# Kernel tuning notes

Hardware: AMD Instinct MI355X
Metric: run time of the kernel (lower is better)

## Reference

```python
import jax, jax.numpy as jnp
import numpy as np
from jax import lax

EPS = 2e-05


def _conv2d(x, w, b, stride):
    # x: [B,C,H,W], w: [O,I,3,3] (OIHW), VALID padding
    y = lax.conv_general_dilated(x, w, (stride, stride), 'VALID',
                                 dimension_numbers=('NCHW', 'OIHW', 'NCHW'))
    return y + b[None, :, None, None]


def _reflect_pad(x):
    return jnp.pad(x, ((0, 0), (0, 0), (1, 1), (1, 1)), mode='reflect')


def _transfer(cont_feat, styl_feat):
    # cont_feat, styl_feat: [B, N, H, W]
    B, N, H, W = cont_feat.shape
    xc = cont_feat.reshape(B, N, -1)   # [B,N,Mc]
    xs = styl_feat.reshape(B, N, -1)   # [B,N,Ms]
    I = jnp.eye(N, dtype=xc.dtype)

    # whitening of content
    mc = jnp.mean(xc, axis=-1, keepdims=True)
    xc0 = xc - mc
    cov_c = jnp.einsum('bnm,bkm->bnk', xc0, xc0) / (xc0.shape[-1] - 1)
    Lc = jnp.linalg.cholesky(cov_c + EPS * I)  # eps*I regularization (torch retry loop)
    inv_Lc = jnp.linalg.inv(Lc)
    whiten = jnp.einsum('bnk,bkm->bnm', inv_Lc, xc0)

    # coloring with style statistics
    ms = jnp.mean(xs, axis=-1, keepdims=True)
    xs0 = xs - ms
    cov_s = jnp.einsum('bnm,bkm->bnk', xs0, xs0) / (xs0.shape[-1] - 1)
    Ls = jnp.linalg.cholesky(cov_s + EPS * I)
    colored = jnp.einsum('bnk,bkm->bnm', Ls, whiten) + ms
    return colored.reshape(B, N, H, W)


def setup_inputs() -> dict:
    key = jax.random.key(0)
    k1, k2, k3, k4 = jax.random.split(key, 4)
    B, C, H, W = 8, 128, 256, 256
    cont_feat = jax.random.normal(k1, (B, C, H, W), dtype=jnp.float32)
    styl_feat = jax.random.normal(k2, (B, C, H, W), dtype=jnp.float32)
    # conv params (kaiming-ish scaling)
    fan1 = C * 9
    W1 = jax.random.normal(k3, (C, C, 3, 3), dtype=jnp.float32) / np.sqrt(fan1)
    b1 = jnp.zeros((C,), dtype=jnp.float32)
    W2 = jax.random.normal(k4, (2 * C, C, 3, 3), dtype=jnp.float32) / np.sqrt(fan1)
    b2 = jnp.zeros((2 * C,), dtype=jnp.float32)
    return {'cont_feat': cont_feat, 'styl_feat': styl_feat,
            'W1': W1, 'b1': b1, 'W2': W2, 'b2': b2}


def reference(cont_feat, styl_feat, W1, b1, W2, b2):
    cs = _transfer(cont_feat, styl_feat)          # [B,C,H,W]
    x = _conv2d(_reflect_pad(cs), W1, b1, 2)      # [B,C,H/2,W/2]
    x = jax.nn.relu(x)
    out = _conv2d(_reflect_pad(x), W2, b2, 1)     # [B,2C,H/2,W/2]
    return out
```

## Files before the change

kernel.cpp:

```cpp
#include <hip/hip_runtime.h>
#include <hip/hip_bf16.h>

#define B_  8
#define C_  128
#define M_  65536
#define EPSV 2e-05f

typedef __attribute__((ext_vector_type(8))) short bf16x8;
typedef __attribute__((ext_vector_type(4))) float f32x4;

#define MFMA(a, b, c) __builtin_amdgcn_mfma_f32_16x16x32_bf16((a), (b), (c), 0, 0, 0)

__device__ __forceinline__ short f2b(float f) {
    unsigned u = __float_as_uint(f);
    u = (u + 0x7FFFu + ((u >> 16) & 1u)) >> 16;
    return (short)u;
}

__device__ __forceinline__ int swz(int px, int c) {
    return px * 256 + ((((c >> 3) ^ (px & 15)) << 4) | ((c & 7) << 1));
}

__device__ __forceinline__ int rot(int i, int k) {
    return i * 128 + ((((k >> 2) + i) & 31) << 2) + (k & 3);
}

__global__ __launch_bounds__(256) void k_prep(const float* W1, const float* W2,
                                              short* wp1, short* wp2) {
    int idx = blockIdx.x * 256 + threadIdx.x;
    if (idx < 9 * 128 * 128) {
        int c = idx & 127, o = (idx >> 7) & 127, rs = idx >> 14;
        wp1[idx] = f2b(W1[(o * 128 + c) * 9 + rs]);
    }
    idx -= 9 * 128 * 128;
    if (idx >= 0 && idx < 9 * 256 * 128) {
        int c = idx & 127, o = (idx >> 7) & 255, rs = idx >> 15;
        wp2[idx] = f2b(W2[(o * 128 + c) * 9 + rs]);
    }
}

__global__ __launch_bounds__(256, 2) void k_gram(const float* cont, const float* styl,
                                                 float* G, float* S) {
    __shared__ short ls[128 * 136];
    __shared__ float ssum[128 * 32];
    int bx = blockIdx.x;
    int chunk = bx & 31, which = (bx >> 5) & 1, b = bx >> 6;
    const float* X = (which ? styl : cont) + (size_t)b * C_ * M_ + chunk * 2048;
    int tid = threadIdx.x, lane = tid & 63, wid = tid >> 6;
    int kg = tid & 31, r0 = tid >> 5;

    float sacc[16];
    #pragma unroll
    for (int p = 0; p < 16; ++p) sacc[p] = 0.f;
    f32x4 acc[2][8];
    for (int u = 0; u < 2; ++u)
        for (int j = 0; j < 8; ++j) acc[u][j] = (f32x4){0.f, 0.f, 0.f, 0.f};

    float4 pf[16];
    #pragma unroll
    for (int p = 0; p < 16; ++p)
        pf[p] = *(const float4*)(X + (size_t)(r0 + p * 8) * M_ + kg * 4);

    for (int it = 0; it < 16; ++it) {
        #pragma unroll
        for (int p = 0; p < 16; ++p) {
            int row = r0 + p * 8;
            float4 v = pf[p];
            sacc[p] += v.x + v.y + v.z + v.w;
            union { __hip_bfloat162 h[2]; unsigned long long u; } pk;
            pk.h[0] = __float22bfloat162_rn(make_float2(v.x, v.y));
            pk.h[1] = __float22bfloat162_rn(make_float2(v.z, v.w));
            *(unsigned long long*)(ls + row * 136 + kg * 4) = pk.u;
        }
        if (it < 15) {
            int kb = (it + 1) * 128;
            #pragma unroll
            for (int p = 0; p < 16; ++p)
                pf[p] = *(const float4*)(X + (size_t)(r0 + p * 8) * M_ + kb + kg * 4);
        }
        asm volatile("s_waitcnt lgkmcnt(0)" ::: "memory");
        __builtin_amdgcn_sched_barrier(0);
        __builtin_amdgcn_s_barrier();
        for (int ks = 0; ks < 4; ++ks) {
            int co = ks * 32 + (lane >> 4) * 8;
            bf16x8 a[2], bbf[8];
            for (int u = 0; u < 2; ++u) {
                int row = (wid * 2 + u) * 16 + (lane & 15);
                a[u] = *(const bf16x8*)(ls + row * 136 + co);
            }
            for (int j = 0; j < 8; ++j) {
                int row = j * 16 + (lane & 15);
                bbf[j] = *(const bf16x8*)(ls + row * 136 + co);
            }
            for (int u = 0; u < 2; ++u)
                for (int j = 0; j < 8; ++j)
                    acc[u][j] = MFMA(a[u], bbf[j], acc[u][j]);
        }
        __builtin_amdgcn_sched_barrier(0);
        __builtin_amdgcn_s_barrier();
    }
    __syncthreads();
    for (int p = 0; p < 16; ++p) ssum[(r0 + p * 8) * 32 + kg] = sacc[p];
    __syncthreads();
    float* Gp = G + ((size_t)which * 8 + b) * 16384;
    float* Sp = S + ((size_t)which * 8 + b) * 128;
    if (tid < 128) {
        float s = 0.f;
        for (int q = 0; q < 32; ++q) s += ssum[tid * 32 + q];
        atomicAdd(&Sp[tid], s);
    }
    for (int u = 0; u < 2; ++u) {
        int rowb = (wid * 2 + u) * 16 + (lane >> 4) * 4;
        for (int j = 0; j < 8; ++j) {
            int col = j * 16 + (lane & 15);
            for (int e = 0; e < 4; ++e)
                atomicAdd(&Gp[(rowb + e) * 128 + col], acc[u][j][e]);
        }
    }
}

__global__ __launch_bounds__(128) void k_chol(const float* G, const float* S,
                                              float* LcT, float* Lsg) {
    __shared__ float A[128 * 128];
    int wb = blockIdx.x;
    int i = threadIdx.x;
    const float invM = 1.f / 65536.f;
    const float invM1 = 1.f / 65535.f;
    const float* Gp = G + (size_t)wb * 16384;
    const float* Sp = S + (size_t)wb * 128;
    float mui = Sp[i] * invM;

    for (int j = 0; j <= i; ++j) {
        float muj = Sp[j] * invM;
        float cv = (Gp[i * 128 + j] - 65536.f * mui * muj) * invM1;
        if (j == i) cv += EPSV;
        A[rot(i, j)] = cv;
    }
    for (int bb = 0; bb < 4; ++bb) {
        int jb0 = bb * 32, bend = jb0 + 32;
        for (int j = jb0; j < bend; ++j) {
            __syncthreads();
            float dot = 0.f;
            if (i >= j) {
                int c0 = jb0 >> 2, c1 = j >> 2;
                float4 dd = {0.f, 0.f, 0.f, 0.f};
                for (int c = c0; c < c1; ++c) {
                    float4 x = *(const float4*)(A + i * 128 + (((c + i) & 31) << 2));
                    float4 y = *(const float4*)(A + j * 128 + (((c + j) & 31) << 2));
                    dd.x += x.x * y.x; dd.y += x.y * y.y;
                    dd.z += x.z * y.z; dd.w += x.w * y.w;
                }
                dot = dd.x + dd.y + dd.z + dd.w;
                for (int k = c1 << 2; k < j; ++k)
                    dot += A[rot(i, k)] * A[rot(j, k)];
            }
            if (i == j) A[127] = sqrtf(A[rot(i, j)] - dot);
            __syncthreads();
            if (i > j)       A[rot(i, j)] = (A[rot(i, j)] - dot) / A[127];
            else if (i == j) A[rot(i, j)] = A[127];
        }
        if (bb < 3) {
            __syncthreads();
            if (i >= bend) {
                float t[32];
                #pragma unroll
                for (int g = 0; g < 8; ++g) {
                    float4 v = *(const float4*)(A + i * 128 +
                                ((((jb0 >> 2) + g + i) & 31) << 2));
                    t[g * 4 + 0] = v.x; t[g * 4 + 1] = v.y;
                    t[g * 4 + 2] = v.z; t[g * 4 + 3] = v.w;
                }
                int jmax = (i & ~63) + 64;
                for (int j4 = bend; j4 < jmax; j4 += 4) {
                    float* rp = A + i * 128 + ((((j4 >> 2) + i) & 31) << 2);
                    float4 r = *(float4*)rp;
                    #pragma unroll
                    for (int g = 0; g < 8; ++g) {
                        int kc = (jb0 >> 2) + g;
                        float4 c0 = *(const float4*)(A + (j4 + 0) * 128 + (((kc + j4 + 0) & 31) << 2));
                        float4 c1 = *(const float4*)(A + (j4 + 1) * 128 + (((kc + j4 + 1) & 31) << 2));
                        float4 c2 = *(const float4*)(A + (j4 + 2) * 128 + (((kc + j4 + 2) & 31) << 2));
                        float4 c3 = *(const float4*)(A + (j4 + 3) * 128 + (((kc + j4 + 3) & 31) << 2));
                        float ta = t[g * 4], tb = t[g * 4 + 1], tc = t[g * 4 + 2], td = t[g * 4 + 3];
                        r.x -= ta * c0.x + tb * c0.y + tc * c0.z + td * c0.w;
                        r.y -= ta * c1.x + tb * c1.y + tc * c1.z + td * c1.w;
                        r.z -= ta * c2.x + tb * c2.y + tc * c2.z + td * c2.w;
                        r.w -= ta * c3.x + tb * c3.y + tc * c3.z + td * c3.w;
                    }
                    *(float4*)rp = r;
                }
            }
        }
    }
    __syncthreads();
    if (wb < 8) {
        float* dst = LcT + (size_t)wb * 16384;
        for (int j = 0; j <= i; ++j)
            dst[j * 128 + i] = A[rot(i, j)];
    } else {
        float4* dst = (float4*)(Lsg + (size_t)(wb - 8) * 16384);
        const float4* src = (const float4*)A;
        for (int t = i; t < 4096; t += 128) dst[t] = src[t];
    }
}

__global__ __launch_bounds__(128) void k_trsm(const float* LcT, const float* Lsg,
                                              const float* S, short* Tb, float* Vv) {
    __shared__ float A[128 * 128];
    int b = blockIdx.x;
    int i = threadIdx.x;
    const float invM = 1.f / 65536.f;
    const float* Lc = LcT + (size_t)b * 16384;
    {
        const float4* src = (const float4*)(Lsg + (size_t)b * 16384);
        float4* dst = (float4*)A;
        for (int t = i; t < 4096; t += 128) dst[t] = src[t];
    }
    __syncthreads();
    float lsdia = A[rot(i, i)];
    float rdia = 1.f / Lc[i * 128 + i];
    float tii = lsdia * rdia;
    __syncthreads();
    for (int j = 0; j < 127; ++j)
        if (i > j) A[rot(j, i)] = Lc[j * 128 + i];
    A[rot(i, i)] = rdia;
    __syncthreads();

    for (int bb = 3; bb >= 0; --bb) {
        int jb0 = bb * 32, bend = jb0 + 32;
        int khi = (i < bend) ? i : bend;
        int jstart = (i < bend) ? (i - 1) : (bend - 1);
        for (int j = jstart; j >= jb0; --j) {
            float dot = (i < bend) ? tii * A[rot(j, i)] : 0.f;
            int k = j + 1;
            int ka = (k + 3) & ~3; if (ka > khi) ka = khi;
            for (; k < ka; ++k) dot += A[rot(i, k)] * A[rot(j, k)];
            for (; k + 3 < khi; k += 4) {
                float4 x = *(const float4*)(A + i * 128 + ((((k >> 2) + i) & 31) << 2));
                float4 y = *(const float4*)(A + j * 128 + ((((k >> 2) + j) & 31) << 2));
                dot += x.x * y.x + x.y * y.y + x.z * y.z + x.w * y.w;
            }
            for (; k < khi; ++k) dot += A[rot(i, k)] * A[rot(j, k)];
            A[rot(i, j)] = (A[rot(i, j)] - dot) * A[rot(j, j)];
        }
        if (jb0 > 0 && i >= jb0) {
            float t[32];
            #pragma unroll
            for (int g = 0; g < 8; ++g) {
                float4 v = *(const float4*)(A + i * 128 +
                            ((((jb0 >> 2) + g + i) & 31) << 2));
                t[g * 4 + 0] = v.x; t[g * 4 + 1] = v.y;
                t[g * 4 + 2] = v.z; t[g * 4 + 3] = v.w;
            }
            if (i < bend) {
                #pragma unroll
                for (int kk = 0; kk < 32; ++kk) {
                    int k = jb0 + kk;
                    if (k == i) t[kk] = tii;
                    else if (k > i) t[kk] = 0.f;
                }
            }
            for (int j4 = 0; j4 < jb0; j4 += 4) {
                float* rp = A + i * 128 + ((((j4 >> 2) + i) & 31) << 2);
                float4 r = *(float4*)rp;
                #pragma unroll
                for (int g = 0; g < 8; ++g) {
                    int kc = (jb0 >> 2) + g;
                    float4 c0 = *(const float4*)(A + (j4 + 0) * 128 + (((kc + j4 + 0) & 31) << 2));
                    float4 c1 = *(const float4*)(A + (j4 + 1) * 128 + (((kc + j4 + 1) & 31) << 2));
                    float4 c2 = *(const float4*)(A + (j4 + 2) * 128 + (((kc + j4 + 2) & 31) << 2));
                    float4 c3 = *(const float4*)(A + (j4 + 3) * 128 + (((kc + j4 + 3) & 31) << 2));
                    float ta = t[g * 4], tb2 = t[g * 4 + 1], tc = t[g * 4 + 2], td = t[g * 4 + 3];
                    r.x -= ta * c0.x + tb2 * c0.y + tc * c0.z + td * c0.w;
                    r.y -= ta * c1.x + tb2 * c1.y + tc * c1.z + td * c1.w;
                    r.z -= ta * c2.x + tb2 * c2.y + tc * c2.z + td * c2.w;
                    r.w -= ta * c3.x + tb2 * c3.y + tc * c3.z + td * c3.w;
                }
                *(float4*)rp = r;
            }
        }
    }
    const float* Sc = S + (size_t)b * 128;
    const float* Ss = S + (size_t)(8 + b) * 128;
    float vdot = 0.f;
    short* Tr = Tb + (size_t)b * 16384 + i * 128;
    for (int j = 0; j < 128; ++j) {
        float t = (j < i) ? A[rot(i, j)] : (j == i ? tii : 0.f);
        Tr[j] = f2b(t);
        if (j <= i) vdot += t * (Sc[j] * invM);
    }
    Vv[b * 128 + i] = Ss[i] * invM - vdot;
}

__global__ __launch_bounds__(256) void k_transform(const float* cont, const short* Tb,
                                                   const float* Vv, short* colored) {
    __shared__ short ls[16384];
    char* lsb = (char*)ls;
    int bx = blockIdx.x;
    int b = bx >> 9, p0 = (bx & 511) << 7;
    int tid = threadIdx.x, lane = tid & 63, wid = tid >> 6;

    {
        int px = tid & 127, ch = tid >> 7;
        const float* Xp = cont + (size_t)b * C_ * M_ + p0 + px;
        for (int it = 0; it < 16; ++it) {
            int c0 = it * 8 + ch * 4;
            float x0 = Xp[(size_t)(c0 + 0) * M_];
            float x1 = Xp[(size_t)(c0 + 1) * M_];
            float x2 = Xp[(size_t)(c0 + 2) * M_];
            float x3 = Xp[(size_t)(c0 + 3) * M_];
            union { short s[4]; unsigned long long u; } pk;
            pk.s[0] = f2b(x0); pk.s[1] = f2b(x1); pk.s[2] = f2b(x2); pk.s[3] = f2b(x3);
            *(unsigned long long*)(lsb + swz(px, c0)) = pk.u;
        }
    }
    __syncthreads();
    f32x4 acc[8][2];
    for (int pg = 0; pg < 8; ++pg)
        for (int u = 0; u < 2; ++u) acc[pg][u] = (f32x4){0.f, 0.f, 0.f, 0.f};
    const short* Tbase = Tb + (size_t)b * 16384;
    for (int kc = 0; kc < 4; ++kc) {
        int co = kc * 32 + (lane >> 4) * 8;
        bf16x8 bfr[2], afr[8];
        for (int u = 0; u < 2; ++u) {
            int chn = (wid * 2 + u) * 16 + (lane & 15);
            bfr[u] = *(const bf16x8*)(Tbase + chn * 128 + co);
        }
        for (int pg = 0; pg < 8; ++pg) {
            int px = pg * 16 + (lane & 15);
            afr[pg] = *(const bf16x8*)(lsb + swz(px, co));
        }
        for (int pg = 0; pg < 8; ++pg)
            for (int u = 0; u < 2; ++u)
                acc[pg][u] = MFMA(afr[pg], bfr[u], acc[pg][u]);
    }
    __syncthreads();
    for (int u = 0; u < 2; ++u) {
        int chn = (wid * 2 + u) * 16 + (lane & 15);
        float vv = Vv[b * 128 + chn];
        for (int pg = 0; pg < 8; ++pg)
            for (int e = 0; e < 4; ++e) {
                int px = pg * 16 + (lane >> 4) * 4 + e;
                *(short*)(lsb + swz(px, chn)) = f2b(acc[pg][u][e] + vv);
            }
    }
    __syncthreads();
    short* dst = colored + ((size_t)b * M_ + p0) * 128;
    for (int it = 0; it < 8; ++it) {
        int gid = tid + it * 256;
        int px = gid >> 4, gr = gid & 15;
        bf16x8 v = *(const bf16x8*)(lsb + px * 256 + ((gr ^ (px & 15)) << 4));
        *(bf16x8*)(dst + (size_t)px * 128 + gr * 8) = v;
    }
}

__global__ __launch_bounds__(256) void k_conv1(const short* colored, const short* wp1,
                                               const float* b1, short* out1) {
    __shared__ short ls[130 * 128];
    char* lsb = (char*)ls;
    int x0 = blockIdx.x * 64, y = blockIdx.y, b = blockIdx.z;
    int tid = threadIdx.x, lane = tid & 63, wid = tid >> 6;

    f32x4 acc[4][2];
    for (int pg = 0; pg < 4; ++pg)
        for (int u = 0; u < 2; ++u) acc[pg][u] = (f32x4){0.f, 0.f, 0.f, 0.f};

    for (int r = 0; r < 3; ++r) {
        int grow = 2 * y - 1 + r;
        if (grow < 0) grow = -grow;
        __syncthreads();
        const short* src = colored + ((size_t)b * M_ + grow * 256) * 128;
        for (int it = 0; it < 9; ++it) {
            int gid = tid + it * 256;
            if (gid < 130 * 16) {
                int L = gid >> 4, gr = gid & 15;
                int gcol = 2 * x0 - 1 + L;
                if (gcol < 0) gcol = -gcol;
                else if (gcol > 255) gcol = 510 - gcol;
                bf16x8 v = *(const bf16x8*)(src + (size_t)gcol * 128 + gr * 8);
                *(bf16x8*)(lsb + L * 256 + ((gr ^ (L & 15)) << 4)) = v;
            }
        }
        __syncthreads();
        for (int s = 0; s < 3; ++s)
            for (int kc = 0; kc < 4; ++kc) {
                int co = kc * 32 + (lane >> 4) * 8;
                bf16x8 afr[4], bfr[2];
                for (int pg = 0; pg < 4; ++pg) {
                    int L = (pg * 16 + (lane & 15)) * 2 + s;
                    afr[pg] = *(const bf16x8*)(lsb + swz(L, co));
                }
                const short* wb = wp1 + (r * 3 + s) * 128 * 128;
                for (int u = 0; u < 2; ++u) {
                    int o = (wid * 2 + u) * 16 + (lane & 15);
                    bfr[u] = *(const bf16x8*)(wb + o * 128 + co);
                }
                for (int pg = 0; pg < 4; ++pg)
                    for (int u = 0; u < 2; ++u)
                        acc[pg][u] = MFMA(afr[pg], bfr[u], acc[pg][u]);
            }
    }
    __syncthreads();
    for (int u = 0; u < 2; ++u) {
        int o = (wid * 2 + u) * 16 + (lane & 15);
        float bias = b1[o];
        for (int pg = 0; pg < 4; ++pg)
            for (int e = 0; e < 4; ++e) {
                int px = pg * 16 + (lane >> 4) * 4 + e;
                float v = acc[pg][u][e] + bias;
                v = v > 0.f ? v : 0.f;
                *(short*)(lsb + swz(px, o)) = f2b(v);
            }
    }
    __syncthreads();
    short* dst = out1 + ((size_t)b * 16384 + y * 128 + x0) * 128;
    for (int it = 0; it < 4; ++it) {
        int gid = tid + it * 256;
        int px = gid >> 4, gr = gid & 15;
        bf16x8 v = *(const bf16x8*)(lsb + px * 256 + ((gr ^ (px & 15)) << 4));
        *(bf16x8*)(dst + (size_t)px * 128 + gr * 8) = v;
    }
}

__global__ __launch_bounds__(256) void k_conv2(const short* out1, const short* wp2,
                                               const float* b2, float* outp) {
    __shared__ short ls[66 * 128];
    char* lsb = (char*)ls;
    int x0 = blockIdx.x * 64, y = blockIdx.y, b = blockIdx.z;
    int tid = threadIdx.x, lane = tid & 63, wid = tid >> 6;

    f32x4 acc[4][4];
    for (int pg = 0; pg < 4; ++pg)
        for (int u = 0; u < 4; ++u) acc[pg][u] = (f32x4){0.f, 0.f, 0.f, 0.f};

    for (int r = 0; r < 3; ++r) {
        int grow = y - 1 + r;
        if (grow < 0) grow = -grow;
        else if (grow > 127) grow = 254 - grow;
        __syncthreads();
        const short* src = out1 + ((size_t)b * 16384 + grow * 128) * 128;
        for (int it = 0; it < 5; ++it) {
            int gid = tid + it * 256;
            if (gid < 66 * 16) {
                int L = gid >> 4, gr = gid & 15;
                int gcol = x0 - 1 + L;
                if (gcol < 0) gcol = -gcol;
                else if (gcol > 127) gcol = 254 - gcol;
                bf16x8 v = *(const bf16x8*)(src + (size_t)gcol * 128 + gr * 8);
                *(bf16x8*)(lsb + L * 256 + ((gr ^ (L & 15)) << 4)) = v;
            }
        }
        __syncthreads();
        for (int s = 0; s < 3; ++s)
            for (int kc = 0; kc < 4; ++kc) {
                int co = kc * 32 + (lane >> 4) * 8;
                bf16x8 afr[4], bfr[4];
                for (int pg = 0; pg < 4; ++pg) {
                    int L = pg * 16 + (lane & 15) + s;
                    afr[pg] = *(const bf16x8*)(lsb + swz(L, co));
                }
                const short* wb = wp2 + (r * 3 + s) * 256 * 128;
                for (int u = 0; u < 4; ++u) {
                    int o = (wid * 4 + u) * 16 + (lane & 15);
                    bfr[u] = *(const bf16x8*)(wb + o * 128 + co);
                }
                for (int pg = 0; pg < 4; ++pg)
                    for (int u = 0; u < 4; ++u)
                        acc[pg][u] = MFMA(afr[pg], bfr[u], acc[pg][u]);
            }
    }
    for (int u = 0; u < 4; ++u) {
        int o = (wid * 4 + u) * 16 + (lane & 15);
        float bias = b2[o];
        float* dst = outp + ((size_t)b * 256 + o) * 16384 + y * 128 + x0;
        for (int pg = 0; pg < 4; ++pg) {
            float4 v;
            v.x = acc[pg][u][0] + bias;
            v.y = acc[pg][u][1] + bias;
            v.z = acc[pg][u][2] + bias;
            v.w = acc[pg][u][3] + bias;
            *(float4*)(dst + pg * 16 + (lane >> 4) * 4) = v;
        }
    }
}

extern "C" void kernel_launch(void* const* d_in, const int* in_sizes, int n_in,
                              void* d_out, int out_size, void* d_ws, size_t ws_size,
                              hipStream_t stream) {
    const float* cont = (const float*)d_in[0];
    const float* styl = (const float*)d_in[1];
    const float* W1 = (const float*)d_in[2];
    const float* b1 = (const float*)d_in[3];
    const float* W2 = (const float*)d_in[4];
    const float* b2 = (const float*)d_in[5];
    float* outp = (float*)d_out;
    char* ws = (char*)d_ws;

    float* G       = (float*)(ws + 0x0);
    float* S       = (float*)(ws + 0x100000);
    float* LcT     = (float*)(ws + 0x110000);
    float* Lsg     = (float*)(ws + 0x190000);
    short* Tb      = (short*)(ws + 0x210000);
    float* Vv      = (float*)(ws + 0x250000);
    short* wp1     = (short*)(ws + 0x260000);
    short* wp2     = (short*)(ws + 0x2A8000);
    short* colored = (short*)(ws + 0x400000);
    short* out1    = (short*)(ws + 0x8400000);

    hipMemsetAsync(G, 0, 0x102000, stream);
    k_prep<<<1728, 256, 0, stream>>>(W1, W2, wp1, wp2);
    k_gram<<<512, 256, 0, stream>>>(cont, styl, G, S);
    k_chol<<<16, 128, 0, stream>>>(G, S, LcT, Lsg);
    k_trsm<<<8, 128, 0, stream>>>(LcT, Lsg, S, Tb, Vv);
    k_transform<<<4096, 256, 0, stream>>>(cont, Tb, Vv, colored);
    k_conv1<<<dim3(2, 128, 8), 256, 0, stream>>>(colored, wp1, b1, out1);
    k_conv2<<<dim3(2, 128, 8), 256, 0, stream>>>(out1, wp2, b2, outp);
}
```

Before: 760.7 us.

## Replace Gram atomics with partial buffers plus reduction; register-blocked Cholesky and TRSM panels

The Gram kernel now writes each chunk's 128x128 partial product to a workspace buffer instead of doing float atomicAdds into G. A new k_gsum kernel sums the 32 chunk partials per matrix. The Cholesky panel factorization and the triangular inverse panels now keep the current 32-column panel in registers, fully unrolled, with one barrier per column instead of two. This removes atomic contention and shortens the serial single-block factorization, at the cost of an extra kernel launch, about 32 MB of partial-buffer traffic, and higher register pressure.

```diff
diff --git a/kernel.cpp b/kernel.cpp
--- a/kernel.cpp
+++ b/kernel.cpp
@@ -40,7 +40,7 @@
 }
 
 __global__ __launch_bounds__(256, 2) void k_gram(const float* cont, const float* styl,
-                                                 float* G, float* S) {
+                                                 float* part, float* S) {
     __shared__ short ls[128 * 136];
     __shared__ float ssum[128 * 32];
     int bx = blockIdx.x;
@@ -102,21 +102,31 @@
     __syncthreads();
     for (int p = 0; p < 16; ++p) ssum[(r0 + p * 8) * 32 + kg] = sacc[p];
     __syncthreads();
-    float* Gp = G + ((size_t)which * 8 + b) * 16384;
     float* Sp = S + ((size_t)which * 8 + b) * 128;
     if (tid < 128) {
         float s = 0.f;
         for (int q = 0; q < 32; ++q) s += ssum[tid * 32 + q];
         atomicAdd(&Sp[tid], s);
     }
+    float* Pp = part + ((size_t)((which * 8 + b) * 32 + chunk)) * 16384;
     for (int u = 0; u < 2; ++u) {
         int rowb = (wid * 2 + u) * 16 + (lane >> 4) * 4;
         for (int j = 0; j < 8; ++j) {
             int col = j * 16 + (lane & 15);
             for (int e = 0; e < 4; ++e)
-                atomicAdd(&Gp[(rowb + e) * 128 + col], acc[u][j][e]);
-        }
-    }
+                Pp[(rowb + e) * 128 + col] = acc[u][j][e];
+        }
+    }
+}
+
+__global__ __launch_bounds__(256) void k_gsum(const float* part, float* G) {
+    int idx = blockIdx.x * 256 + threadIdx.x;
+    int m = idx >> 14, e = idx & 16383;
+    const float* p = part + (size_t)m * 32 * 16384 + e;
+    float s = 0.f;
+    #pragma unroll
+    for (int c = 0; c < 32; ++c) s += p[(size_t)c * 16384];
+    G[idx] = s;
 }
 
 __global__ __launch_bounds__(128) void k_chol(const float* G, const float* S,
@@ -136,44 +146,43 @@
         if (j == i) cv += EPSV;
         A[rot(i, j)] = cv;
     }
+    __syncthreads();
+
+    #pragma unroll
     for (int bb = 0; bb < 4; ++bb) {
-        int jb0 = bb * 32, bend = jb0 + 32;
-        for (int j = jb0; j < bend; ++j) {
+        const int jb0 = bb * 32, bend = jb0 + 32;
+        float t[32], u[32], t0[32];
+        #pragma unroll
+        for (int kk = 0; kk < 32; ++kk) t0[kk] = A[rot(i, jb0 + kk)];
+        #pragma unroll
+        for (int jj = 0; jj < 32; ++jj) {
+            const int j = jb0 + jj;
+            float dot = 0.f;
+            #pragma unroll
+            for (int kk = 0; kk < jj; ++kk)
+                dot += u[kk] * A[rot(j, jb0 + kk)];
+            float raw = t0[jj] - dot;
+            if (i >= j) A[rot(i, j)] = raw;
             __syncthreads();
-            float dot = 0.f;
-            if (i >= j) {
-                int c0 = jb0 >> 2, c1 = j >> 2;
-                float4 dd = {0.f, 0.f, 0.f, 0.f};
-                for (int c = c0; c < c1; ++c) {
-                    float4 x = *(const float4*)(A + i * 128 + (((c + i) & 31) << 2));
-                    float4 y = *(const float4*)(A + j * 128 + (((c + j) & 31) << 2));
-                    dd.x += x.x * y.x; dd.y += x.y * y.y;
-                    dd.z += x.z * y.z; dd.w += x.w * y.w;
-                }
-                dot = dd.x + dd.y + dd.z + dd.w;
-                for (int k = c1 << 2; k < j; ++k)
-                    dot += A[rot(i, k)] * A[rot(j, k)];
-            }
-            if (i == j) A[127] = sqrtf(A[rot(i, j)] - dot);
-            __syncthreads();
-            if (i > j)       A[rot(i, j)] = (A[rot(i, j)] - dot) / A[127];
-            else if (i == j) A[rot(i, j)] = A[127];
-        }
+            float pr = A[rot(j, j)];
+            float piv = sqrtf(pr);
+            float rpj = 1.f / piv;
+            float tv = (i > j) ? raw * rpj : (i == j ? piv : 0.f);
+            t[jj] = tv;
+            u[jj] = tv * rpj;
+        }
+        #pragma unroll
+        for (int kk = 0; kk < 32; ++kk) {
+            int j = jb0 + kk;
+            if (i >= j) A[rot(i, j)] = t[kk];
+        }
+        __syncthreads();
         if (bb < 3) {
-            __syncthreads();
             if (i >= bend) {
-                float t[32];
-                #pragma unroll
-                for (int g = 0; g < 8; ++g) {
-                    float4 v = *(const float4*)(A + i * 128 +
-                                ((((jb0 >> 2) + g + i) & 31) << 2));
-                    t[g * 4 + 0] = v.x; t[g * 4 + 1] = v.y;
-                    t[g * 4 + 2] = v.z; t[g * 4 + 3] = v.w;
-                }
                 int jmax = (i & ~63) + 64;
                 for (int j4 = bend; j4 < jmax; j4 += 4) {
-                    float* rp = A + i * 128 + ((((j4 >> 2) + i) & 31) << 2);
-                    float4 r = *(float4*)rp;
+                    float* rp_ = A + i * 128 + ((((j4 >> 2) + i) & 31) << 2);
+                    float4 r = *(float4*)rp_;
                     #pragma unroll
                     for (int g = 0; g < 8; ++g) {
                         int kc = (jb0 >> 2) + g;
@@ -187,9 +196,10 @@
                         r.z -= ta * c2.x + tb * c2.y + tc * c2.z + td * c2.w;
                         r.w -= ta * c3.x + tb * c3.y + tc * c3.z + td * c3.w;
                     }
-                    *(float4*)rp = r;
+                    *(float4*)rp_ = r;
                 }
             }
+            __syncthreads();
         }
     }
     __syncthreads();
@@ -226,40 +236,29 @@
     A[rot(i, i)] = rdia;
     __syncthreads();
 
+    #pragma unroll
     for (int bb = 3; bb >= 0; --bb) {
-        int jb0 = bb * 32, bend = jb0 + 32;
-        int khi = (i < bend) ? i : bend;
-        int jstart = (i < bend) ? (i - 1) : (bend - 1);
-        for (int j = jstart; j >= jb0; --j) {
+        const int jb0 = bb * 32, bend = jb0 + 32;
+        float t[32], ls0[32];
+        #pragma unroll
+        for (int kk = 0; kk < 32; ++kk) ls0[kk] = A[rot(i, jb0 + kk)];
+        #pragma unroll
+        for (int jj = 31; jj >= 0; --jj) {
+            const int j = jb0 + jj;
             float dot = (i < bend) ? tii * A[rot(j, i)] : 0.f;
-            int k = j + 1;
-            int ka = (k + 3) & ~3; if (ka > khi) ka = khi;
-            for (; k < ka; ++k) dot += A[rot(i, k)] * A[rot(j, k)];
-            for (; k + 3 < khi; k += 4) {
-                float4 x = *(const float4*)(A + i * 128 + ((((k >> 2) + i) & 31) << 2));
-                float4 y = *(const float4*)(A + j * 128 + ((((k >> 2) + j) & 31) << 2));
-                dot += x.x * y.x + x.y * y.y + x.z * y.z + x.w * y.w;
-            }
-            for (; k < khi; ++k) dot += A[rot(i, k)] * A[rot(j, k)];
-            A[rot(i, j)] = (A[rot(i, j)] - dot) * A[rot(j, j)];
+            #pragma unroll
+            for (int kk = jj + 1; kk < 32; ++kk)
+                dot += t[kk] * A[rot(j, jb0 + kk)];
+            float val = (ls0[jj] - dot) * A[rot(j, j)];
+            t[jj] = (j < i) ? val : 0.f;
+        }
+        #pragma unroll
+        for (int kk = 0; kk < 32; ++kk) {
+            int j = jb0 + kk;
+            if (j < i) A[rot(i, j)] = t[kk];
+            if (j == i) t[kk] = tii;
         }
         if (jb0 > 0 && i >= jb0) {
-            float t[32];
-            #pragma unroll
-            for (int g = 0; g < 8; ++g) {
-                float4 v = *(const float4*)(A + i * 128 +
-                            ((((jb0 >> 2) + g + i) & 31) << 2));
-                t[g * 4 + 0] = v.x; t[g * 4 + 1] = v.y;
-                t[g * 4 + 2] = v.z; t[g * 4 + 3] = v.w;
-            }
-            if (i < bend) {
-                #pragma unroll
-                for (int kk = 0; kk < 32; ++kk) {
-                    int k = jb0 + kk;
-                    if (k == i) t[kk] = tii;
-                    else if (k > i) t[kk] = 0.f;
-                }
-            }
             for (int j4 = 0; j4 < jb0; j4 += 4) {
                 float* rp = A + i * 128 + ((((j4 >> 2) + i) & 31) << 2);
                 float4 r = *(float4*)rp;
@@ -505,11 +504,13 @@
     short* wp1     = (short*)(ws + 0x260000);
     short* wp2     = (short*)(ws + 0x2A8000);
     short* colored = (short*)(ws + 0x400000);
+    float* part    = (float*)(ws + 0x400000);
     short* out1    = (short*)(ws + 0x8400000);
 
-    hipMemsetAsync(G, 0, 0x102000, stream);
+    hipMemsetAsync(S, 0, 0x2000, stream);
     k_prep<<<1728, 256, 0, stream>>>(W1, W2, wp1, wp2);
-    k_gram<<<512, 256, 0, stream>>>(cont, styl, G, S);
+    k_gram<<<512, 256, 0, stream>>>(cont, styl, part, S);
+    k_gsum<<<1024, 256, 0, stream>>>(part, G);
     k_chol<<<16, 128, 0, stream>>>(G, S, LcT, Lsg);
     k_trsm<<<8, 128, 0, stream>>>(LcT, Lsg, S, Tb, Vv);
     k_transform<<<4096, 256, 0, stream>>>(cont, Tb, Vv, colored);
```

After: 755.3 us. About the same (-0.7%).
